# Performance work log

Measured on AMD Instinct MI355X. Metric: run time of the kernel, lower is better.

## Reference

```python
import jax, jax.numpy as jnp
import numpy as np

N_LAYERS = 3
N_NODES = 512
D_IN = 4  # dimensions + 1
BATCH = 131072


def _glorot(key, shape):
    fan_in, fan_out = shape[-2], shape[-1]
    lim = np.sqrt(6.0 / (fan_in + fan_out))
    return jax.random.uniform(key, shape, jnp.float32, -lim, lim)


def setup_inputs() -> dict:
    key = jax.random.key(0)
    ks = jax.random.split(key, 12)
    L, n, d = N_LAYERS, N_NODES, D_IN
    return {
        "X": jax.random.normal(ks[0], (BATCH, d), jnp.float32),
        "W_in": _glorot(ks[1], (d, n)),
        "b_in": jnp.zeros((1, n), jnp.float32),
        "Wf": _glorot(ks[2], (L, d, n)),
        "Uf": _glorot(ks[3], (L, n, n)),
        "bf": jnp.zeros((L, 1, n), jnp.float32),
        "Wu": _glorot(ks[4], (L, d, n)),
        "Uu": _glorot(ks[5], (L, n, n)),
        "bu": jnp.zeros((L, 1, n), jnp.float32),
        "Wo1": _glorot(ks[6], (L, d, n)),
        "Uo1": _glorot(ks[7], (L, n, n)),
        "bo1": jnp.zeros((L, 1, n), jnp.float32),
        "Wo2": _glorot(ks[8], (L, n, n)),
        "bo2": jnp.zeros((L, 1, n), jnp.float32),
        "W_out": _glorot(ks[9], (n, 1)),
        "b_out": jnp.zeros((1, 1), jnp.float32),
    }


def reference(X, W_in, b_in, Wf, Uf, bf, Wu, Uu, bu, Wo1, Uo1, bo1, Wo2, bo2, W_out, b_out):
    # initial dense layer with swish activation
    H = jax.nn.silu(X @ W_in + b_in)  # [B, n_nodes]
    for i in range(N_LAYERS):
        F = jax.nn.sigmoid(X @ Wf[i] + H @ Uf[i] + bf[i])
        U = jax.nn.sigmoid(X @ Wu[i] + H @ Uu[i] + bu[i])
        O1 = jnp.tanh(X @ Wo1[i] + H @ Uo1[i] + bo1[i])
        O2 = jax.nn.silu((U * O1) @ Wo2[i] + bo2[i])
        H = F * H + O2
    return jax.nn.silu(H @ W_out + b_out)  # [B, 1]
```

## Files before the change

### kernel.cpp

```cpp
#include <hip/hip_runtime.h>
#include <cstdint>
#include <cstddef>

#define NLAYERS 3
#define NN      512
#define DIN     4
#define MTILE   64
#define KAUG    544
#define LDA     552
#define WELEMS  (NN * KAUG)
#define LDS_BYTES (2 * MTILE * LDA * 2)
#define NTHREADS 1024

typedef __attribute__((ext_vector_type(8))) short short8;
typedef __attribute__((ext_vector_type(4))) float f32x4;

__device__ __forceinline__ short f2bf(float f) {
    union { float f; uint32_t u; } v; v.f = f;
    uint32_t r = v.u + 0x7fffu + ((v.u >> 16) & 1u);
    return (short)(r >> 16);
}
__device__ __forceinline__ float bf2f(short s) {
    union { uint32_t u; float f; } v; v.u = ((uint32_t)(uint16_t)s) << 16;
    return v.f;
}
__device__ __forceinline__ float sig_(float x)  { return 1.0f / (1.0f + __expf(-x)); }
__device__ __forceinline__ float tanh_(float x) { return 1.0f - 2.0f / (1.0f + __expf(2.0f * x)); }
__device__ __forceinline__ float silu_(float x) { return x / (1.0f + __expf(-x)); }

__global__ void prep_kernel(const float* __restrict__ Wf,  const float* __restrict__ Uf,  const float* __restrict__ bf,
                            const float* __restrict__ Wu,  const float* __restrict__ Uu,  const float* __restrict__ bu,
                            const float* __restrict__ Wo1, const float* __restrict__ Uo1, const float* __restrict__ bo1,
                            const float* __restrict__ Wo2, const float* __restrict__ bo2,
                            short* __restrict__ ws) {
    int idx = blockIdx.x * 256 + threadIdx.x;
    int m   = idx / WELEMS;
    if (m >= 12) return;
    int rem = idx - m * WELEMS;
    int n   = rem / KAUG;
    int kk  = rem - n * KAUG;
    int layer = m >> 2, t = m & 3;
    const float* U; const float* W; const float* b;
    switch (t) {
        case 0:  U = Uf;  W = Wf;      b = bf;  break;
        case 1:  U = Uu;  W = Wu;      b = bu;  break;
        case 2:  U = Uo1; W = Wo1;     b = bo1; break;
        default: U = Wo2; W = nullptr; b = bo2; break;
    }
    float val = 0.0f;
    if (kk < NN)             val = U[layer * NN * NN + kk * NN + n];
    else if (kk < NN + DIN)  val = W ? W[layer * DIN * NN + (kk - NN) * NN + n] : 0.0f;
    else if (kk == NN + DIN) val = b[layer * NN + n];
    ws[idx] = f2bf(val);
}

__device__ __forceinline__ void mm1(const short* __restrict__ Asrc, const short* __restrict__ Bt,
                                    int n0, int l16, int quad, f32x4 (&acc)[4][2]) {
#pragma unroll
    for (int mt = 0; mt < 4; ++mt)
#pragma unroll
        for (int nt = 0; nt < 2; ++nt) acc[mt][nt] = f32x4{0.f, 0.f, 0.f, 0.f};
    const short* aP = Asrc + l16 * LDA + quad * 8;
    const short* bP = Bt + (size_t)(n0 + l16) * KAUG + quad * 8;

    short8 aA[4], bA[2], aB[4], bB[2];
#pragma unroll
    for (int mt = 0; mt < 4; ++mt) aA[mt] = *(const short8*)(aP + mt * 16 * LDA);
    bA[0] = *(const short8*)(bP);
    bA[1] = *(const short8*)(bP + 16 * KAUG);

#pragma unroll 1
    for (int i = 0; i < 8; ++i) {
#pragma unroll
        for (int mt = 0; mt < 4; ++mt) aB[mt] = *(const short8*)(aP + mt * 16 * LDA + 32);
        bB[0] = *(const short8*)(bP + 32);
        bB[1] = *(const short8*)(bP + 16 * KAUG + 32);
#pragma unroll
        for (int mt = 0; mt < 4; ++mt) {
            acc[mt][0] = __builtin_amdgcn_mfma_f32_16x16x32_bf16(aA[mt], bA[0], acc[mt][0], 0, 0, 0);
            acc[mt][1] = __builtin_amdgcn_mfma_f32_16x16x32_bf16(aA[mt], bA[1], acc[mt][1], 0, 0, 0);
        }
#pragma unroll
        for (int mt = 0; mt < 4; ++mt) aA[mt] = *(const short8*)(aP + mt * 16 * LDA + 64);
        bA[0] = *(const short8*)(bP + 64);
        bA[1] = *(const short8*)(bP + 16 * KAUG + 64);
#pragma unroll
        for (int mt = 0; mt < 4; ++mt) {
            acc[mt][0] = __builtin_amdgcn_mfma_f32_16x16x32_bf16(aB[mt], bB[0], acc[mt][0], 0, 0, 0);
            acc[mt][1] = __builtin_amdgcn_mfma_f32_16x16x32_bf16(aB[mt], bB[1], acc[mt][1], 0, 0, 0);
        }
        aP += 64; bP += 64;
    }
#pragma unroll
    for (int mt = 0; mt < 4; ++mt) {
        acc[mt][0] = __builtin_amdgcn_mfma_f32_16x16x32_bf16(aA[mt], bA[0], acc[mt][0], 0, 0, 0);
        acc[mt][1] = __builtin_amdgcn_mfma_f32_16x16x32_bf16(aA[mt], bA[1], acc[mt][1], 0, 0, 0);
    }
}

__global__ void __launch_bounds__(NTHREADS, 4)
dgm_kernel(const float* __restrict__ X, const float* __restrict__ W_in, const float* __restrict__ b_in,
           const float* __restrict__ W_out, const float* __restrict__ b_out,
           const short* __restrict__ wmats, float* __restrict__ out) {
    extern __shared__ short lds[];
    short* Hb = lds;
    short* Tb = lds + MTILE * LDA;

    const int tid  = threadIdx.x;
    const int lane = tid & 63;
    const int wv   = tid >> 6;
    const int l16  = lane & 15;
    const int quad = lane >> 4;
    const int n0   = wv * 32;
    const int rbase = blockIdx.x * MTILE;

#pragma unroll 4
    for (int j = 0; j < (MTILE * NN) / NTHREADS; ++j) {
        int idx = tid + j * NTHREADS;
        int r = idx >> 9;
        int c = idx & (NN - 1);
        const float* xr = X + (size_t)(rbase + r) * DIN;
        float v = b_in[c];
#pragma unroll
        for (int k = 0; k < DIN; ++k) v += xr[k] * W_in[k * NN + c];
        Hb[r * LDA + c] = f2bf(silu_(v));
    }
    if (tid < MTILE) {
        int r = tid;
        const float* xr = X + (size_t)(rbase + r) * DIN;
#pragma unroll
        for (int k = 0; k < DIN; ++k) {
            Hb[r * LDA + NN + k] = f2bf(xr[k]);
            Tb[r * LDA + NN + k] = 0;
        }
        Hb[r * LDA + NN + DIN] = f2bf(1.0f);
        Tb[r * LDA + NN + DIN] = f2bf(1.0f);
        for (int k = NN + DIN + 1; k < KAUG; ++k) {
            Hb[r * LDA + k] = 0;
            Tb[r * LDA + k] = 0;
        }
    }
    __syncthreads();

    uint32_t Fpack[16];

    for (int layer = 0; layer < NLAYERS; ++layer) {
        const short* wF  = wmats + (size_t)(layer * 4 + 0) * WELEMS;
        const short* wU  = wmats + (size_t)(layer * 4 + 1) * WELEMS;
        const short* wO1 = wmats + (size_t)(layer * 4 + 2) * WELEMS;
        const short* wO2 = wmats + (size_t)(layer * 4 + 3) * WELEMS;

        uint32_t Tpack[16];
        {
            f32x4 aO[4][2];
            mm1(Hb, wO1, n0, l16, quad, aO);
#pragma unroll
            for (int mt = 0; mt < 4; ++mt)
#pragma unroll
                for (int nt = 0; nt < 2; ++nt)
#pragma unroll
                    for (int rp = 0; rp < 2; ++rp) {
                        uint32_t lo = (uint16_t)f2bf(tanh_(aO[mt][nt][2 * rp + 0]));
                        uint32_t hi = (uint16_t)f2bf(tanh_(aO[mt][nt][2 * rp + 1]));
                        Tpack[mt * 4 + nt * 2 + rp] = lo | (hi << 16);
                    }
        }
        {
            f32x4 aU[4][2];
            mm1(Hb, wU, n0, l16, quad, aU);
#pragma unroll
            for (int mt = 0; mt < 4; ++mt)
#pragma unroll
                for (int nt = 0; nt < 2; ++nt)
#pragma unroll
                    for (int rg = 0; rg < 4; ++rg) {
                        uint32_t tp = Tpack[mt * 4 + nt * 2 + (rg >> 1)];
                        float to = bf2f((short)(uint16_t)((rg & 1) ? (tp >> 16) : (tp & 0xffffu)));
                        int row = mt * 16 + quad * 4 + rg;
                        int col = n0 + nt * 16 + l16;
                        Tb[row * LDA + col] = f2bf(sig_(aU[mt][nt][rg]) * to);
                    }
        }
        {
            f32x4 aF[4][2];
            mm1(Hb, wF, n0, l16, quad, aF);
#pragma unroll
            for (int mt = 0; mt < 4; ++mt)
#pragma unroll
                for (int nt = 0; nt < 2; ++nt)
#pragma unroll
                    for (int rp = 0; rp < 2; ++rp) {
                        uint32_t lo = (uint16_t)f2bf(sig_(aF[mt][nt][2 * rp + 0]));
                        uint32_t hi = (uint16_t)f2bf(sig_(aF[mt][nt][2 * rp + 1]));
                        Fpack[mt * 4 + nt * 2 + rp] = lo | (hi << 16);
                    }
        }
        __syncthreads();

        {
            f32x4 aO2[4][2];
            mm1(Tb, wO2, n0, l16, quad, aO2);
#pragma unroll
            for (int mt = 0; mt < 4; ++mt)
#pragma unroll
                for (int nt = 0; nt < 2; ++nt)
#pragma unroll
                    for (int rg = 0; rg < 4; ++rg) {
                        uint32_t fp = Fpack[mt * 4 + nt * 2 + (rg >> 1)];
                        float f = bf2f((short)(uint16_t)((rg & 1) ? (fp >> 16) : (fp & 0xffffu)));
                        int row = mt * 16 + quad * 4 + rg;
                        int col = n0 + nt * 16 + l16;
                        float hold = bf2f(Hb[row * LDA + col]);
                        float o2 = silu_(aO2[mt][nt][rg]);
                        Hb[row * LDA + col] = f2bf(f * hold + o2);
                    }
        }
        __syncthreads();
    }

    {
        const int r = tid >> 4, q = tid & 15;
        const int c0 = q * (NN / 16);
        float p = 0.0f;
        for (int c = c0; c < c0 + NN / 16; ++c)
            p += bf2f(Hb[r * LDA + c]) * W_out[c];
        float* red = (float*)Tb;
        red[tid] = p;
        __syncthreads();
        if (q == 0) {
            float s = b_out[0];
#pragma unroll
            for (int i = 0; i < 16; ++i) s += red[r * 16 + i];
            out[rbase + r] = silu_(s);
        }
    }
}

extern "C" void kernel_launch(void* const* d_in, const int* in_sizes, int n_in,
                              void* d_out, int out_size, void* d_ws, size_t ws_size,
                              hipStream_t stream) {
    const float* X     = (const float*)d_in[0];
    const float* W_in  = (const float*)d_in[1];
    const float* b_in  = (const float*)d_in[2];
    const float* Wf    = (const float*)d_in[3];
    const float* Uf    = (const float*)d_in[4];
    const float* bf    = (const float*)d_in[5];
    const float* Wu    = (const float*)d_in[6];
    const float* Uu    = (const float*)d_in[7];
    const float* bu    = (const float*)d_in[8];
    const float* Wo1   = (const float*)d_in[9];
    const float* Uo1   = (const float*)d_in[10];
    const float* bo1   = (const float*)d_in[11];
    const float* Wo2   = (const float*)d_in[12];
    const float* bo2   = (const float*)d_in[13];
    const float* W_out = (const float*)d_in[14];
    const float* b_out = (const float*)d_in[15];
    float* out = (float*)d_out;
    short* ws  = (short*)d_ws;

    const int B = in_sizes[0] / DIN;

    prep_kernel<<<(12 * WELEMS + 255) / 256, 256, 0, stream>>>(
        Wf, Uf, bf, Wu, Uu, bu, Wo1, Uo1, bo1, Wo2, bo2, ws);

    hipFuncSetAttribute((const void*)dgm_kernel,
                        hipFuncAttributeMaxDynamicSharedMemorySize, LDS_BYTES);
    dgm_kernel<<<B / MTILE, NTHREADS, LDS_BYTES, stream>>>(X, W_in, b_in, W_out, b_out, ws, out);
}
```

Baseline: 1.319 ms.

## Widen per-wave N tile to 64 columns with 512-thread blocks

```diff
diff --git a/kernel.cpp b/kernel.cpp
--- a/kernel.cpp
+++ b/kernel.cpp
@@ -10,7 +10,7 @@
 #define LDA     552
 #define WELEMS  (NN * KAUG)
 #define LDS_BYTES (2 * MTILE * LDA * 2)
-#define NTHREADS 1024
+#define NTHREADS 512
 
 typedef __attribute__((ext_vector_type(8))) short short8;
 typedef __attribute__((ext_vector_type(4))) float f32x4;
@@ -54,51 +54,51 @@
     ws[idx] = f2bf(val);
 }
 
-__device__ __forceinline__ void mm1(const short* __restrict__ Asrc, const short* __restrict__ Bt,
-                                    int n0, int l16, int quad, f32x4 (&acc)[4][2]) {
+__device__ __forceinline__ void mm2(const short* __restrict__ Asrc, const short* __restrict__ Bt,
+                                    int n0, int l16, int quad, f32x4 (&acc)[4][4]) {
 #pragma unroll
     for (int mt = 0; mt < 4; ++mt)
 #pragma unroll
-        for (int nt = 0; nt < 2; ++nt) acc[mt][nt] = f32x4{0.f, 0.f, 0.f, 0.f};
+        for (int nt = 0; nt < 4; ++nt) acc[mt][nt] = f32x4{0.f, 0.f, 0.f, 0.f};
     const short* aP = Asrc + l16 * LDA + quad * 8;
     const short* bP = Bt + (size_t)(n0 + l16) * KAUG + quad * 8;
 
-    short8 aA[4], bA[2], aB[4], bB[2];
+    short8 aA[4], bA[4], aB[4], bB[4];
 #pragma unroll
     for (int mt = 0; mt < 4; ++mt) aA[mt] = *(const short8*)(aP + mt * 16 * LDA);
-    bA[0] = *(const short8*)(bP);
-    bA[1] = *(const short8*)(bP + 16 * KAUG);
+#pragma unroll
+    for (int nt = 0; nt < 4; ++nt) bA[nt] = *(const short8*)(bP + nt * 16 * KAUG);
 
 #pragma unroll 1
     for (int i = 0; i < 8; ++i) {
 #pragma unroll
         for (int mt = 0; mt < 4; ++mt) aB[mt] = *(const short8*)(aP + mt * 16 * LDA + 32);
-        bB[0] = *(const short8*)(bP + 32);
-        bB[1] = *(const short8*)(bP + 16 * KAUG + 32);
-#pragma unroll
-        for (int mt = 0; mt < 4; ++mt) {
-            acc[mt][0] = __builtin_amdgcn_mfma_f32_16x16x32_bf16(aA[mt], bA[0], acc[mt][0], 0, 0, 0);
-            acc[mt][1] = __builtin_amdgcn_mfma_f32_16x16x32_bf16(aA[mt], bA[1], acc[mt][1], 0, 0, 0);
-        }
+#pragma unroll
+        for (int nt = 0; nt < 4; ++nt) bB[nt] = *(const short8*)(bP + nt * 16 * KAUG + 32);
+#pragma unroll
+        for (int mt = 0; mt < 4; ++mt)
+#pragma unroll
+            for (int nt = 0; nt < 4; ++nt)
+                acc[mt][nt] = __builtin_amdgcn_mfma_f32_16x16x32_bf16(aA[mt], bA[nt], acc[mt][nt], 0, 0, 0);
 #pragma unroll
         for (int mt = 0; mt < 4; ++mt) aA[mt] = *(const short8*)(aP + mt * 16 * LDA + 64);
-        bA[0] = *(const short8*)(bP + 64);
-        bA[1] = *(const short8*)(bP + 16 * KAUG + 64);
-#pragma unroll
-        for (int mt = 0; mt < 4; ++mt) {
-            acc[mt][0] = __builtin_amdgcn_mfma_f32_16x16x32_bf16(aB[mt], bB[0], acc[mt][0], 0, 0, 0);
-            acc[mt][1] = __builtin_amdgcn_mfma_f32_16x16x32_bf16(aB[mt], bB[1], acc[mt][1], 0, 0, 0);
-        }
+#pragma unroll
+        for (int nt = 0; nt < 4; ++nt) bA[nt] = *(const short8*)(bP + nt * 16 * KAUG + 64);
+#pragma unroll
+        for (int mt = 0; mt < 4; ++mt)
+#pragma unroll
+            for (int nt = 0; nt < 4; ++nt)
+                acc[mt][nt] = __builtin_amdgcn_mfma_f32_16x16x32_bf16(aB[mt], bB[nt], acc[mt][nt], 0, 0, 0);
         aP += 64; bP += 64;
     }
 #pragma unroll
-    for (int mt = 0; mt < 4; ++mt) {
-        acc[mt][0] = __builtin_amdgcn_mfma_f32_16x16x32_bf16(aA[mt], bA[0], acc[mt][0], 0, 0, 0);
-        acc[mt][1] = __builtin_amdgcn_mfma_f32_16x16x32_bf16(aA[mt], bA[1], acc[mt][1], 0, 0, 0);
-    }
-}
-
-__global__ void __launch_bounds__(NTHREADS, 4)
+    for (int mt = 0; mt < 4; ++mt)
+#pragma unroll
+        for (int nt = 0; nt < 4; ++nt)
+            acc[mt][nt] = __builtin_amdgcn_mfma_f32_16x16x32_bf16(aA[mt], bA[nt], acc[mt][nt], 0, 0, 0);
+}
+
+__global__ void __launch_bounds__(NTHREADS, 2)
 dgm_kernel(const float* __restrict__ X, const float* __restrict__ W_in, const float* __restrict__ b_in,
            const float* __restrict__ W_out, const float* __restrict__ b_out,
            const short* __restrict__ wmats, float* __restrict__ out) {
@@ -111,7 +111,7 @@
     const int wv   = tid >> 6;
     const int l16  = lane & 15;
     const int quad = lane >> 4;
-    const int n0   = wv * 32;
+    const int n0   = wv * 64;
     const int rbase = blockIdx.x * MTILE;
 
 #pragma unroll 4
@@ -142,7 +142,7 @@
     }
     __syncthreads();
 
-    uint32_t Fpack[16];
+    uint32_t Fpack[32];
 
     for (int layer = 0; layer < NLAYERS; ++layer) {
         const short* wF  = wmats + (size_t)(layer * 4 + 0) * WELEMS;
@@ -150,31 +150,31 @@
         const short* wO1 = wmats + (size_t)(layer * 4 + 2) * WELEMS;
         const short* wO2 = wmats + (size_t)(layer * 4 + 3) * WELEMS;
 
-        uint32_t Tpack[16];
-        {
-            f32x4 aO[4][2];
-            mm1(Hb, wO1, n0, l16, quad, aO);
-#pragma unroll
-            for (int mt = 0; mt < 4; ++mt)
-#pragma unroll
-                for (int nt = 0; nt < 2; ++nt)
+        uint32_t Tpack[32];
+        {
+            f32x4 aO[4][4];
+            mm2(Hb, wO1, n0, l16, quad, aO);
+#pragma unroll
+            for (int mt = 0; mt < 4; ++mt)
+#pragma unroll
+                for (int nt = 0; nt < 4; ++nt)
 #pragma unroll
                     for (int rp = 0; rp < 2; ++rp) {
                         uint32_t lo = (uint16_t)f2bf(tanh_(aO[mt][nt][2 * rp + 0]));
                         uint32_t hi = (uint16_t)f2bf(tanh_(aO[mt][nt][2 * rp + 1]));
-                        Tpack[mt * 4 + nt * 2 + rp] = lo | (hi << 16);
-                    }
-        }
-        {
-            f32x4 aU[4][2];
-            mm1(Hb, wU, n0, l16, quad, aU);
-#pragma unroll
-            for (int mt = 0; mt < 4; ++mt)
-#pragma unroll
-                for (int nt = 0; nt < 2; ++nt)
+                        Tpack[mt * 8 + nt * 2 + rp] = lo | (hi << 16);
+                    }
+        }
+        {
+            f32x4 aU[4][4];
+            mm2(Hb, wU, n0, l16, quad, aU);
+#pragma unroll
+            for (int mt = 0; mt < 4; ++mt)
+#pragma unroll
+                for (int nt = 0; nt < 4; ++nt)
 #pragma unroll
                     for (int rg = 0; rg < 4; ++rg) {
-                        uint32_t tp = Tpack[mt * 4 + nt * 2 + (rg >> 1)];
+                        uint32_t tp = Tpack[mt * 8 + nt * 2 + (rg >> 1)];
                         float to = bf2f((short)(uint16_t)((rg & 1) ? (tp >> 16) : (tp & 0xffffu)));
                         int row = mt * 16 + quad * 4 + rg;
                         int col = n0 + nt * 16 + l16;
@@ -182,31 +182,31 @@
                     }
         }
         {
-            f32x4 aF[4][2];
-            mm1(Hb, wF, n0, l16, quad, aF);
-#pragma unroll
-            for (int mt = 0; mt < 4; ++mt)
-#pragma unroll
-                for (int nt = 0; nt < 2; ++nt)
+            f32x4 aF[4][4];
+            mm2(Hb, wF, n0, l16, quad, aF);
+#pragma unroll
+            for (int mt = 0; mt < 4; ++mt)
+#pragma unroll
+                for (int nt = 0; nt < 4; ++nt)
 #pragma unroll
                     for (int rp = 0; rp < 2; ++rp) {
                         uint32_t lo = (uint16_t)f2bf(sig_(aF[mt][nt][2 * rp + 0]));
                         uint32_t hi = (uint16_t)f2bf(sig_(aF[mt][nt][2 * rp + 1]));
-                        Fpack[mt * 4 + nt * 2 + rp] = lo | (hi << 16);
+                        Fpack[mt * 8 + nt * 2 + rp] = lo | (hi << 16);
                     }
         }
         __syncthreads();
 
         {
-            f32x4 aO2[4][2];
-            mm1(Tb, wO2, n0, l16, quad, aO2);
-#pragma unroll
-            for (int mt = 0; mt < 4; ++mt)
-#pragma unroll
-                for (int nt = 0; nt < 2; ++nt)
+            f32x4 aO2[4][4];
+            mm2(Tb, wO2, n0, l16, quad, aO2);
+#pragma unroll
+            for (int mt = 0; mt < 4; ++mt)
+#pragma unroll
+                for (int nt = 0; nt < 4; ++nt)
 #pragma unroll
                     for (int rg = 0; rg < 4; ++rg) {
-                        uint32_t fp = Fpack[mt * 4 + nt * 2 + (rg >> 1)];
+                        uint32_t fp = Fpack[mt * 8 + nt * 2 + (rg >> 1)];
                         float f = bf2f((short)(uint16_t)((rg & 1) ? (fp >> 16) : (fp & 0xffffu)));
                         int row = mt * 16 + quad * 4 + rg;
                         int col = n0 + nt * 16 + l16;
@@ -219,10 +219,10 @@
     }
 
     {
-        const int r = tid >> 4, q = tid & 15;
-        const int c0 = q * (NN / 16);
+        const int r = tid >> 3, q = tid & 7;
+        const int c0 = q * (NN / 8);
         float p = 0.0f;
-        for (int c = c0; c < c0 + NN / 16; ++c)
+        for (int c = c0; c < c0 + NN / 8; ++c)
             p += bf2f(Hb[r * LDA + c]) * W_out[c];
         float* red = (float*)Tb;
         red[tid] = p;
@@ -230,7 +230,7 @@
         if (q == 0) {
             float s = b_out[0];
 #pragma unroll
-            for (int i = 0; i < 16; ++i) s += red[r * 16 + i];
+            for (int i = 0; i < 8; ++i) s += red[r * 8 + i];
             out[rbase + r] = silu_(s);
         }
     }
```

New measurement: 1.414 ms. 7.1% more time.

## Halve row tile, swizzle LDS layout, and stage tanh output through LDS

Applied to the files above, without the earlier changes.

```diff
diff --git a/kernel.cpp b/kernel.cpp
--- a/kernel.cpp
+++ b/kernel.cpp
@@ -5,12 +5,14 @@
 #define NLAYERS 3
 #define NN      512
 #define DIN     4
-#define MTILE   64
+#define MTILE   32
 #define KAUG    544
 #define LDA     552
 #define WELEMS  (NN * KAUG)
 #define LDS_BYTES (2 * MTILE * LDA * 2)
 #define NTHREADS 1024
+
+#define SWZ(r, c) ((c) ^ ((r) & 8))
 
 typedef __attribute__((ext_vector_type(8))) short short8;
 typedef __attribute__((ext_vector_type(4))) float f32x4;
@@ -55,50 +57,50 @@
 }
 
 __device__ __forceinline__ void mm1(const short* __restrict__ Asrc, const short* __restrict__ Bt,
-                                    int n0, int l16, int quad, f32x4 (&acc)[4][2]) {
-#pragma unroll
-    for (int mt = 0; mt < 4; ++mt)
+                                    int n0, int l16, int quad, f32x4 (&acc)[2][2]) {
+#pragma unroll
+    for (int mt = 0; mt < 2; ++mt)
 #pragma unroll
         for (int nt = 0; nt < 2; ++nt) acc[mt][nt] = f32x4{0.f, 0.f, 0.f, 0.f};
-    const short* aP = Asrc + l16 * LDA + quad * 8;
+    const short* aP = Asrc + l16 * LDA + (((quad * 8) ^ (l16 & 8)));
     const short* bP = Bt + (size_t)(n0 + l16) * KAUG + quad * 8;
 
-    short8 aA[4], bA[2], aB[4], bB[2];
-#pragma unroll
-    for (int mt = 0; mt < 4; ++mt) aA[mt] = *(const short8*)(aP + mt * 16 * LDA);
-    bA[0] = *(const short8*)(bP);
-    bA[1] = *(const short8*)(bP + 16 * KAUG);
+    short8 a0[2], a1[2], b0[2], b1[2];
+#pragma unroll
+    for (int mt = 0; mt < 2; ++mt) a0[mt] = *(const short8*)(aP + mt * 16 * LDA);
+#pragma unroll
+    for (int nt = 0; nt < 2; ++nt) b0[nt] = *(const short8*)(bP + nt * 16 * KAUG);
 
 #pragma unroll 1
     for (int i = 0; i < 8; ++i) {
 #pragma unroll
-        for (int mt = 0; mt < 4; ++mt) aB[mt] = *(const short8*)(aP + mt * 16 * LDA + 32);
-        bB[0] = *(const short8*)(bP + 32);
-        bB[1] = *(const short8*)(bP + 16 * KAUG + 32);
-#pragma unroll
-        for (int mt = 0; mt < 4; ++mt) {
-            acc[mt][0] = __builtin_amdgcn_mfma_f32_16x16x32_bf16(aA[mt], bA[0], acc[mt][0], 0, 0, 0);
-            acc[mt][1] = __builtin_amdgcn_mfma_f32_16x16x32_bf16(aA[mt], bA[1], acc[mt][1], 0, 0, 0);
-        }
-#pragma unroll
-        for (int mt = 0; mt < 4; ++mt) aA[mt] = *(const short8*)(aP + mt * 16 * LDA + 64);
-        bA[0] = *(const short8*)(bP + 64);
-        bA[1] = *(const short8*)(bP + 16 * KAUG + 64);
-#pragma unroll
-        for (int mt = 0; mt < 4; ++mt) {
-            acc[mt][0] = __builtin_amdgcn_mfma_f32_16x16x32_bf16(aB[mt], bB[0], acc[mt][0], 0, 0, 0);
-            acc[mt][1] = __builtin_amdgcn_mfma_f32_16x16x32_bf16(aB[mt], bB[1], acc[mt][1], 0, 0, 0);
-        }
+        for (int mt = 0; mt < 2; ++mt) a1[mt] = *(const short8*)(aP + mt * 16 * LDA + 32);
+#pragma unroll
+        for (int nt = 0; nt < 2; ++nt) b1[nt] = *(const short8*)(bP + nt * 16 * KAUG + 32);
+#pragma unroll
+        for (int mt = 0; mt < 2; ++mt)
+#pragma unroll
+            for (int nt = 0; nt < 2; ++nt)
+                acc[mt][nt] = __builtin_amdgcn_mfma_f32_16x16x32_bf16(a0[mt], b0[nt], acc[mt][nt], 0, 0, 0);
+#pragma unroll
+        for (int mt = 0; mt < 2; ++mt) a0[mt] = *(const short8*)(aP + mt * 16 * LDA + 64);
+#pragma unroll
+        for (int nt = 0; nt < 2; ++nt) b0[nt] = *(const short8*)(bP + nt * 16 * KAUG + 64);
+#pragma unroll
+        for (int mt = 0; mt < 2; ++mt)
+#pragma unroll
+            for (int nt = 0; nt < 2; ++nt)
+                acc[mt][nt] = __builtin_amdgcn_mfma_f32_16x16x32_bf16(a1[mt], b1[nt], acc[mt][nt], 0, 0, 0);
         aP += 64; bP += 64;
     }
 #pragma unroll
-    for (int mt = 0; mt < 4; ++mt) {
-        acc[mt][0] = __builtin_amdgcn_mfma_f32_16x16x32_bf16(aA[mt], bA[0], acc[mt][0], 0, 0, 0);
-        acc[mt][1] = __builtin_amdgcn_mfma_f32_16x16x32_bf16(aA[mt], bA[1], acc[mt][1], 0, 0, 0);
-    }
-}
-
-__global__ void __launch_bounds__(NTHREADS, 4)
+    for (int mt = 0; mt < 2; ++mt)
+#pragma unroll
+        for (int nt = 0; nt < 2; ++nt)
+            acc[mt][nt] = __builtin_amdgcn_mfma_f32_16x16x32_bf16(a0[mt], b0[nt], acc[mt][nt], 0, 0, 0);
+}
+
+__global__ void __launch_bounds__(NTHREADS, 8)
 dgm_kernel(const float* __restrict__ X, const float* __restrict__ W_in, const float* __restrict__ b_in,
            const float* __restrict__ W_out, const float* __restrict__ b_out,
            const short* __restrict__ wmats, float* __restrict__ out) {
@@ -123,26 +125,26 @@
         float v = b_in[c];
 #pragma unroll
         for (int k = 0; k < DIN; ++k) v += xr[k] * W_in[k * NN + c];
-        Hb[r * LDA + c] = f2bf(silu_(v));
+        Hb[r * LDA + SWZ(r, c)] = f2bf(silu_(v));
     }
     if (tid < MTILE) {
         int r = tid;
         const float* xr = X + (size_t)(rbase + r) * DIN;
 #pragma unroll
         for (int k = 0; k < DIN; ++k) {
-            Hb[r * LDA + NN + k] = f2bf(xr[k]);
-            Tb[r * LDA + NN + k] = 0;
-        }
-        Hb[r * LDA + NN + DIN] = f2bf(1.0f);
-        Tb[r * LDA + NN + DIN] = f2bf(1.0f);
+            Hb[r * LDA + SWZ(r, NN + k)] = f2bf(xr[k]);
+            Tb[r * LDA + SWZ(r, NN + k)] = 0;
+        }
+        Hb[r * LDA + SWZ(r, NN + DIN)] = f2bf(1.0f);
+        Tb[r * LDA + SWZ(r, NN + DIN)] = f2bf(1.0f);
         for (int k = NN + DIN + 1; k < KAUG; ++k) {
-            Hb[r * LDA + k] = 0;
-            Tb[r * LDA + k] = 0;
+            Hb[r * LDA + SWZ(r, k)] = 0;
+            Tb[r * LDA + SWZ(r, k)] = 0;
         }
     }
     __syncthreads();
 
-    uint32_t Fpack[16];
+    uint32_t Fpack[8];
 
     for (int layer = 0; layer < NLAYERS; ++layer) {
         const short* wF  = wmats + (size_t)(layer * 4 + 0) * WELEMS;
@@ -150,42 +152,41 @@
         const short* wO1 = wmats + (size_t)(layer * 4 + 2) * WELEMS;
         const short* wO2 = wmats + (size_t)(layer * 4 + 3) * WELEMS;
 
-        uint32_t Tpack[16];
-        {
-            f32x4 aO[4][2];
+        {
+            f32x4 aO[2][2];
             mm1(Hb, wO1, n0, l16, quad, aO);
 #pragma unroll
-            for (int mt = 0; mt < 4; ++mt)
-#pragma unroll
-                for (int nt = 0; nt < 2; ++nt)
-#pragma unroll
-                    for (int rp = 0; rp < 2; ++rp) {
-                        uint32_t lo = (uint16_t)f2bf(tanh_(aO[mt][nt][2 * rp + 0]));
-                        uint32_t hi = (uint16_t)f2bf(tanh_(aO[mt][nt][2 * rp + 1]));
-                        Tpack[mt * 4 + nt * 2 + rp] = lo | (hi << 16);
-                    }
-        }
-        {
-            f32x4 aU[4][2];
-            mm1(Hb, wU, n0, l16, quad, aU);
-#pragma unroll
-            for (int mt = 0; mt < 4; ++mt)
+            for (int mt = 0; mt < 2; ++mt)
 #pragma unroll
                 for (int nt = 0; nt < 2; ++nt)
 #pragma unroll
                     for (int rg = 0; rg < 4; ++rg) {
-                        uint32_t tp = Tpack[mt * 4 + nt * 2 + (rg >> 1)];
-                        float to = bf2f((short)(uint16_t)((rg & 1) ? (tp >> 16) : (tp & 0xffffu)));
                         int row = mt * 16 + quad * 4 + rg;
                         int col = n0 + nt * 16 + l16;
-                        Tb[row * LDA + col] = f2bf(sig_(aU[mt][nt][rg]) * to);
-                    }
-        }
-        {
-            f32x4 aF[4][2];
+                        Tb[row * LDA + SWZ(row, col)] = f2bf(tanh_(aO[mt][nt][rg]));
+                    }
+        }
+        {
+            f32x4 aU[2][2];
+            mm1(Hb, wU, n0, l16, quad, aU);
+#pragma unroll
+            for (int mt = 0; mt < 2; ++mt)
+#pragma unroll
+                for (int nt = 0; nt < 2; ++nt)
+#pragma unroll
+                    for (int rg = 0; rg < 4; ++rg) {
+                        int row = mt * 16 + quad * 4 + rg;
+                        int col = n0 + nt * 16 + l16;
+                        int off = row * LDA + SWZ(row, col);
+                        float to = bf2f(Tb[off]);
+                        Tb[off] = f2bf(sig_(aU[mt][nt][rg]) * to);
+                    }
+        }
+        {
+            f32x4 aF[2][2];
             mm1(Hb, wF, n0, l16, quad, aF);
 #pragma unroll
-            for (int mt = 0; mt < 4; ++mt)
+            for (int mt = 0; mt < 2; ++mt)
 #pragma unroll
                 for (int nt = 0; nt < 2; ++nt)
 #pragma unroll
@@ -198,10 +199,10 @@
         __syncthreads();
 
         {
-            f32x4 aO2[4][2];
+            f32x4 aO2[2][2];
             mm1(Tb, wO2, n0, l16, quad, aO2);
 #pragma unroll
-            for (int mt = 0; mt < 4; ++mt)
+            for (int mt = 0; mt < 2; ++mt)
 #pragma unroll
                 for (int nt = 0; nt < 2; ++nt)
 #pragma unroll
@@ -210,27 +211,28 @@
                         float f = bf2f((short)(uint16_t)((rg & 1) ? (fp >> 16) : (fp & 0xffffu)));
                         int row = mt * 16 + quad * 4 + rg;
                         int col = n0 + nt * 16 + l16;
-                        float hold = bf2f(Hb[row * LDA + col]);
+                        int off = row * LDA + SWZ(row, col);
+                        float hold = bf2f(Hb[off]);
                         float o2 = silu_(aO2[mt][nt][rg]);
-                        Hb[row * LDA + col] = f2bf(f * hold + o2);
+                        Hb[off] = f2bf(f * hold + o2);
                     }
         }
         __syncthreads();
     }
 
     {
-        const int r = tid >> 4, q = tid & 15;
-        const int c0 = q * (NN / 16);
+        const int r = tid >> 5, q = tid & 31;
+        const int c0 = q * (NN / 32);
         float p = 0.0f;
-        for (int c = c0; c < c0 + NN / 16; ++c)
-            p += bf2f(Hb[r * LDA + c]) * W_out[c];
+        for (int c = c0; c < c0 + NN / 32; ++c)
+            p += bf2f(Hb[r * LDA + SWZ(r, c)]) * W_out[c];
         float* red = (float*)Tb;
         red[tid] = p;
         __syncthreads();
         if (q == 0) {
             float s = b_out[0];
 #pragma unroll
-            for (int i = 0; i < 16; ++i) s += red[r * 16 + i];
+            for (int i = 0; i < 32; ++i) s += red[r * 32 + i];
             out[rbase + r] = silu_(s);
         }
     }
```

Result: slower. 1.923 ms (+45.8%).
